# Kernel tuning notes

Measured on AMD Instinct MI355X. Metric: run time of the kernel, lower is better.

Reference implementation:

```python
import jax, jax.numpy as jnp
import numpy as np


def _conv3x3(x, w, stride=1):
    # x: [N, C_in, H, W], w: [C_out, C_in, 3, 3] (ternary {-1,0,1}), padding=1, no bias
    return jax.lax.conv_general_dilated(
        x, w,
        window_strides=(stride, stride),
        padding=((1, 1), (1, 1)),
        dimension_numbers=("NCHW", "OIHW", "NCHW"),
    )


def _bn(x, gamma, beta, mean, var, eps=1e-5):
    # inference-mode BatchNorm2d over channel dim
    inv = gamma * jax.lax.rsqrt(var + eps)
    return x * inv[None, :, None, None] + (beta - mean * inv)[None, :, None, None]


def setup_inputs() -> dict:
    key = jax.random.key(0)
    ks = jax.random.split(key, 8)
    N, C, H, W = 64, 256, 32, 32
    x = jax.random.normal(ks[0], (N, C, H, W), dtype=jnp.float32)
    # Ternary conv weights in {-1, 0, +1} (scale_and_shift=False => raw ternary values)
    w1 = jax.random.randint(ks[1], (C, C, 3, 3), -1, 2).astype(jnp.float32)
    w2 = jax.random.randint(ks[2], (C, C, 3, 3), -1, 2).astype(jnp.float32)
    # BatchNorm affine params and running stats
    g1 = jax.random.normal(ks[3], (C,), dtype=jnp.float32) * 0.1 + 1.0
    b1 = jax.random.normal(ks[4], (C,), dtype=jnp.float32) * 0.1
    g2 = jax.random.normal(ks[5], (C,), dtype=jnp.float32) * 0.1 + 1.0
    b2 = jax.random.normal(ks[6], (C,), dtype=jnp.float32) * 0.1
    rm1 = jnp.zeros((C,), dtype=jnp.float32)
    rv1 = jnp.ones((C,), dtype=jnp.float32)
    rm2 = jnp.zeros((C,), dtype=jnp.float32)
    rv2 = jnp.ones((C,), dtype=jnp.float32)
    return {"x": x, "w1": w1, "g1": g1, "b1": b1, "rm1": rm1, "rv1": rv1,
            "w2": w2, "g2": g2, "b2": b2, "rm2": rm2, "rv2": rv2}


def reference(x, w1, g1, b1, rm1, rv1, w2, g2, b2, rm2, rv2):
    # BasicBlock forward: stride=1, downsample=None -> identity skip
    h = _conv3x3(x, w1, stride=1)
    h = _bn(h, g1, b1, rm1, rv1)
    h = jax.nn.relu(h)
    h = _conv3x3(h, w2, stride=1)
    h = _bn(h, g2, b2, rm2, rv2)
    return jax.nn.relu(x + h)
```

## Files before the change

kernel.cpp:

```cpp
#include <hip/hip_runtime.h>

typedef unsigned short u16;
typedef unsigned int u32;
typedef __attribute__((ext_vector_type(8))) short bf16x8;
typedef __attribute__((ext_vector_type(4))) float f32x4;

__device__ __forceinline__ u16 f2bf(float f) {
    u32 u = __float_as_uint(f);
    u += 0x7fffu + ((u >> 16) & 1u);
    return (u16)(u >> 16);
}

__device__ __forceinline__ void llds16(void* l, const void* g) {
    __builtin_amdgcn_global_load_lds(
        (const __attribute__((address_space(1))) u32*)g,
        (__attribute__((address_space(3))) u32*)l, 16, 0, 0);
}

__global__ void prep(const float* __restrict__ x, u16* __restrict__ xt,
                     const float* __restrict__ w1, const float* __restrict__ w2,
                     u16* __restrict__ W1t, u16* __restrict__ W2t,
                     const float* __restrict__ g1, const float* __restrict__ b1,
                     const float* __restrict__ rm1, const float* __restrict__ rv1,
                     const float* __restrict__ g2, const float* __restrict__ b2,
                     const float* __restrict__ rm2, const float* __restrict__ rv2,
                     float* __restrict__ sc, u32* __restrict__ zp) {
    int t = threadIdx.x;
    int b = blockIdx.x;
    if (b < 16384) {
        __shared__ float xl[32 * 33];
        int n = b >> 8, rem = b & 255;
        int h = rem >> 3, c0 = (rem & 7) << 5;
        int cl = t >> 5, w = t & 31;
#pragma unroll
        for (int i = 0; i < 4; ++i) {
            int c = c0 + i * 8 + cl;
            xl[(i * 8 + cl) * 33 + w] = x[(n * 256 + c) * 1024 + h * 32 + w];
        }
        __syncthreads();
        int wo = t >> 3, k = t & 7;
        ushort4 o;
        o.x = f2bf(xl[(k * 4 + 0) * 33 + wo]);
        o.y = f2bf(xl[(k * 4 + 1) * 33 + wo]);
        o.z = f2bf(xl[(k * 4 + 2) * 33 + wo]);
        o.w = f2bf(xl[(k * 4 + 3) * 33 + wo]);
        *(ushort4*)&xt[((n * 32 + h) * 32 + wo) * 256 + c0 + k * 4] = o;
    } else {
        int bb = b - 16384;
        int idx = (bb & 255) * 256 + t;
        const float* src = (bb >> 8) ? w2 : w1;
        u16* dst = (bb >> 8) ? W2t : W1t;
        const float* s = src + idx * 9;
        int co = idx >> 8, ci = idx & 255;
#pragma unroll
        for (int p = 0; p < 9; ++p)
            dst[p * 65536 + co * 256 + ci] = f2bf(s[p]);
        if (bb == 0) {
            float s1 = g1[t] * rsqrtf(rv1[t] + 1e-5f);
            sc[t]       = s1;
            sc[256 + t] = b1[t] - rm1[t] * s1;
            float s2 = g2[t] * rsqrtf(rv2[t] + 1e-5f);
            sc[512 + t] = s2;
            sc[768 + t] = b2[t] - rm2[t] * s2;
            zp[t] = 0u;
            zp[t + 256] = 0u;
        }
    }
}

__global__ __launch_bounds__(512, 1) void conv_mfma(
    const u16* __restrict__ Xt,
    const u16* __restrict__ Wt,
    const float* __restrict__ sv,
    const float* __restrict__ tv,
    const float* __restrict__ skip,
    u16* __restrict__ ybf,
    float* __restrict__ yf,
    const u16* __restrict__ zp, int stage)
{
    __shared__ alignas(16) u16 ldsA[2][9 * 4 * 64 * 8];
    __shared__ alignas(16) u16 ldsB[2][40 * 64 * 8];

    int t = threadIdx.x;
    int wv = t >> 6, lane = t & 63;
    int q = lane >> 4, n16 = lane & 15;

    int bid = blockIdx.x;
    int co_t = (bid >> 3) & 3;
    int sp   = ((bid >> 5) << 3) | (bid & 7);
    int h_t  = sp & 1, nb = sp >> 1;
    int co0 = co_t << 6, h0 = h_t << 4;

    const u16* src[10];
    u32 dstOff[10];
    bool isB = (wv < 4);
    int nld = isB ? 10 : 9;
    if (isB) {
#pragma unroll
        for (int j = 0; j < 10; ++j) {
            int g2 = wv * 10 + j;
            int s = g2 * 64 + lane;
            int hi = s / 136, rem = s - hi * 136;
            int wp = rem >> 2, qq = rem & 3;
            int hin = h0 - 1 + hi;
            bool v = (wp >= 1) && (wp <= 32) && (hin >= 0) && (hin < 32);
            src[j] = v ? (Xt + (((nb << 5) + hin) * 32 + (wp - 1)) * 256 + (qq << 3))
                       : (zp + lane * 8);
            dstOff[j] = (u32)g2 << 9;
        }
    } else {
#pragma unroll
        for (int i = 0; i < 9; ++i) {
            int g = (wv - 4) * 9 + i;
            int p = g >> 2, mt = g & 3;
            src[i] = Wt + (p << 16) + ((co0 + (mt << 4) + n16) << 8) + (q << 3);
            dstOff[i] = (u32)g << 9;
        }
        src[9] = zp; dstOff[9] = 0;
    }

    f32x4 acc[4][4] = {};

    {
        u16* dst = isB ? ldsB[0] : ldsA[0];
#pragma unroll
        for (int j = 0; j < 10; ++j)
            if (j < nld) llds16(&dst[dstOff[j]], src[j]);
    }

    int c = 0;
    for (int kt = 0; kt < 8; ++kt) {
        if (kt < 7) {
            int kc = (kt + 1) << 5;
            u16* dst = isB ? ldsB[c ^ 1] : ldsA[c ^ 1];
#pragma unroll
            for (int j = 0; j < 10; ++j)
                if (j < nld) llds16(&dst[dstOff[j]], src[j] + kc);
            if (isB) asm volatile("s_waitcnt vmcnt(10)" ::: "memory");
            else     asm volatile("s_waitcnt vmcnt(9)"  ::: "memory");
        } else {
            asm volatile("s_waitcnt vmcnt(0)" ::: "memory");
        }
        __builtin_amdgcn_s_barrier();
        __builtin_amdgcn_sched_barrier(0);

        const u16* pA = ldsA[c];
        const u16* pB = ldsB[c];
        __builtin_amdgcn_s_setprio(1);
#pragma unroll
        for (int kw = 0; kw < 3; ++kw) {
            bf16x8 bFr[4][2];
#pragma unroll
            for (int r = 0; r < 4; ++r)
#pragma unroll
                for (int half = 0; half < 2; ++half) {
                    int hi = (wv << 1) + r;
                    int wp = (half << 4) + n16 + kw;
                    bFr[r][half] = *(const bf16x8*)
                        &pB[(hi * 136 + (wp << 2) + q) << 3];
                }
#pragma unroll
            for (int kh = 0; kh < 3; ++kh) {
                int p = kh * 3 + kw;
                bf16x8 aF[4];
#pragma unroll
                for (int mt = 0; mt < 4; ++mt)
                    aF[mt] = *(const bf16x8*)&pA[((p << 8) + (mt << 6) + lane) << 3];
#pragma unroll
                for (int mt = 0; mt < 4; ++mt)
#pragma unroll
                    for (int nt = 0; nt < 4; ++nt)
                        acc[mt][nt] = __builtin_amdgcn_mfma_f32_16x16x32_bf16(
                            aF[mt], bFr[(nt >> 1) + kh][nt & 1], acc[mt][nt], 0, 0, 0);
            }
        }
        __builtin_amdgcn_s_setprio(0);
        __builtin_amdgcn_sched_barrier(0);
        __builtin_amdgcn_s_barrier();
        c ^= 1;
    }

    if (stage == 1) {
#pragma unroll
        for (int mt = 0; mt < 4; ++mt) {
            int cb = co0 + (mt << 4) + (q << 2);
            f32x4 ss = *(const f32x4*)&sv[cb];
            f32x4 tt = *(const f32x4*)&tv[cb];
#pragma unroll
            for (int nt = 0; nt < 4; ++nt) {
                int h = h0 + (wv << 1) + (nt >> 1), w = ((nt & 1) << 4) + n16;
                ushort4 o;
                o.x = f2bf(fmaxf(acc[mt][nt][0] * ss[0] + tt[0], 0.f));
                o.y = f2bf(fmaxf(acc[mt][nt][1] * ss[1] + tt[1], 0.f));
                o.z = f2bf(fmaxf(acc[mt][nt][2] * ss[2] + tt[2], 0.f));
                o.w = f2bf(fmaxf(acc[mt][nt][3] * ss[3] + tt[3], 0.f));
                *(ushort4*)&ybf[(((nb << 5) + h) * 32 + w) * 256 + cb] = o;
            }
        }
    } else {
#pragma unroll
        for (int mt = 0; mt < 4; ++mt) {
            int cb = co0 + (mt << 4) + (q << 2);
            f32x4 ss = *(const f32x4*)&sv[cb];
            f32x4 tt = *(const f32x4*)&tv[cb];
#pragma unroll
            for (int nt = 0; nt < 4; ++nt) {
                int h = h0 + (wv << 1) + (nt >> 1), w = ((nt & 1) << 4) + n16;
#pragma unroll
                for (int j = 0; j < 4; ++j) {
                    int idx = (((nb << 8) + cb + j) << 10) + (h << 5) + w;
                    yf[idx] = fmaxf(acc[mt][nt][j] * ss[j] + tt[j] + skip[idx], 0.f);
                }
            }
        }
    }
}

extern "C" void kernel_launch(void* const* d_in, const int* in_sizes, int n_in,
                              void* d_out, int out_size, void* d_ws, size_t ws_size,
                              hipStream_t stream) {
    const float* x   = (const float*)d_in[0];
    const float* w1  = (const float*)d_in[1];
    const float* g1  = (const float*)d_in[2];
    const float* b1  = (const float*)d_in[3];
    const float* rm1 = (const float*)d_in[4];
    const float* rv1 = (const float*)d_in[5];
    const float* w2  = (const float*)d_in[6];
    const float* g2  = (const float*)d_in[7];
    const float* b2  = (const float*)d_in[8];
    const float* rm2 = (const float*)d_in[9];
    const float* rv2 = (const float*)d_in[10];

    char* ws = (char*)d_ws;
    u16*  XT  = (u16*)(ws);
    u16*  H1  = (u16*)(ws + 33554432);
    u16*  W1t = (u16*)(ws + 67108864);
    u16*  W2t = (u16*)(ws + 68288512);
    float* sc = (float*)(ws + 69468160);
    u32*  zpg = (u32*)(ws + 69472256);
    if (ws_size < 69474304) return;

    prep<<<16896, 256, 0, stream>>>(x, XT, w1, w2, W1t, W2t,
                                    g1, b1, rm1, rv1, g2, b2, rm2, rv2,
                                    sc, zpg);

    conv_mfma<<<512, 512, 0, stream>>>(XT, W1t, sc, sc + 256, nullptr,
                                       H1, nullptr, (const u16*)zpg, 1);
    conv_mfma<<<512, 512, 0, stream>>>(H1, W2t, sc + 512, sc + 768, x,
                                       nullptr, (float*)d_out, (const u16*)zpg, 2);
}
```

Measured before the change: 272.6 us.

## Interleave LDS prefetch with per-tap MFMA phases and allow two blocks per CU

Restructures the K loop into nine per-tap phases. Each phase loads A/B fragments, issues part of the next tile's global-to-LDS prefetch, then runs a barrier-fenced MFMA cluster, which spreads load issue across the compute. Launch bounds move to two blocks per CU to raise occupancy. The price is two extra barriers per tap, a full vmcnt(0) wait at each k-tile start, and register pressure from the occupancy target that could cause spills.

```diff
diff --git a/kernel.cpp b/kernel.cpp
--- a/kernel.cpp
+++ b/kernel.cpp
@@ -68,7 +68,7 @@
     }
 }
 
-__global__ __launch_bounds__(512, 1) void conv_mfma(
+__global__ __launch_bounds__(512, 2) void conv_mfma(
     const u16* __restrict__ Xt,
     const u16* __restrict__ Wt,
     const float* __restrict__ sv,
@@ -130,53 +130,60 @@
 
     int c = 0;
     for (int kt = 0; kt < 8; ++kt) {
-        if (kt < 7) {
-            int kc = (kt + 1) << 5;
-            u16* dst = isB ? ldsB[c ^ 1] : ldsA[c ^ 1];
-#pragma unroll
-            for (int j = 0; j < 10; ++j)
-                if (j < nld) llds16(&dst[dstOff[j]], src[j] + kc);
-            if (isB) asm volatile("s_waitcnt vmcnt(10)" ::: "memory");
-            else     asm volatile("s_waitcnt vmcnt(9)"  ::: "memory");
-        } else {
-            asm volatile("s_waitcnt vmcnt(0)" ::: "memory");
-        }
+        asm volatile("s_waitcnt vmcnt(0)" ::: "memory");
         __builtin_amdgcn_s_barrier();
-        __builtin_amdgcn_sched_barrier(0);
 
         const u16* pA = ldsA[c];
         const u16* pB = ldsB[c];
-        __builtin_amdgcn_s_setprio(1);
-#pragma unroll
-        for (int kw = 0; kw < 3; ++kw) {
-            bf16x8 bFr[4][2];
-#pragma unroll
-            for (int r = 0; r < 4; ++r)
-#pragma unroll
-                for (int half = 0; half < 2; ++half) {
-                    int hi = (wv << 1) + r;
-                    int wp = (half << 4) + n16 + kw;
-                    bFr[r][half] = *(const bf16x8*)
-                        &pB[(hi * 136 + (wp << 2) + q) << 3];
+        u16* dstS = isB ? ldsB[c ^ 1] : ldsA[c ^ 1];
+        int kc = (kt + 1) << 5;
+        bool pf = (kt < 7);
+
+        bf16x8 Bf[4][2];
+
+#pragma unroll
+        for (int tp = 0; tp < 9; ++tp) {
+            const int kw = tp / 3, kh = tp % 3;
+            const int p = kh * 3 + kw;
+            if (kh == 0) {
+#pragma unroll
+                for (int r = 0; r < 4; ++r)
+#pragma unroll
+                    for (int hf = 0; hf < 2; ++hf)
+                        Bf[r][hf] = *(const bf16x8*)
+                            &pB[((wv * 2 + r) * 136 +
+                                 (((hf << 4) + n16 + kw) << 2) + q) << 3];
+            }
+            bf16x8 Af[4];
+#pragma unroll
+            for (int mt = 0; mt < 4; ++mt)
+                Af[mt] = *(const bf16x8*)&pA[((p << 8) + (mt << 6) + lane) << 3];
+
+            if (pf && tp < 5) {
+#pragma unroll
+                for (int u = 0; u < 2; ++u) {
+                    int j = tp * 2 + u;
+                    if (j < 10) {
+                        bool go = (j < nld);
+                        if (go) llds16(&dstS[dstOff[j]], src[j] + kc);
+                    }
                 }
-#pragma unroll
-            for (int kh = 0; kh < 3; ++kh) {
-                int p = kh * 3 + kw;
-                bf16x8 aF[4];
-#pragma unroll
-                for (int mt = 0; mt < 4; ++mt)
-                    aF[mt] = *(const bf16x8*)&pA[((p << 8) + (mt << 6) + lane) << 3];
-#pragma unroll
-                for (int mt = 0; mt < 4; ++mt)
-#pragma unroll
-                    for (int nt = 0; nt < 4; ++nt)
-                        acc[mt][nt] = __builtin_amdgcn_mfma_f32_16x16x32_bf16(
-                            aF[mt], bFr[(nt >> 1) + kh][nt & 1], acc[mt][nt], 0, 0, 0);
-            }
-        }
-        __builtin_amdgcn_s_setprio(0);
-        __builtin_amdgcn_sched_barrier(0);
-        __builtin_amdgcn_s_barrier();
+            }
+
+            __builtin_amdgcn_s_barrier();
+            asm volatile("s_waitcnt lgkmcnt(0)" ::: "memory");
+            __builtin_amdgcn_sched_barrier(0);
+            __builtin_amdgcn_s_setprio(1);
+#pragma unroll
+            for (int mt = 0; mt < 4; ++mt)
+#pragma unroll
+                for (int nt = 0; nt < 4; ++nt)
+                    acc[mt][nt] = __builtin_amdgcn_mfma_f32_16x16x32_bf16(
+                        Af[mt], Bf[(nt >> 1) + kh][nt & 1], acc[mt][nt], 0, 0, 0);
+            __builtin_amdgcn_s_setprio(0);
+            __builtin_amdgcn_sched_barrier(0);
+            __builtin_amdgcn_s_barrier();
+        }
         c ^= 1;
     }
 
```

Result: no change. 275.4 us (+1.0%).

## Restructure conv K-loop: single barrier, prefetch after barrier, double-buffered LDS fragment reads

Applied to the files above, without the earlier changes.

The main loop now waits for all outstanding loads and uses one barrier per iteration instead of two. The next tile's global-to-LDS prefetch is issued after that barrier, into the buffer that was just released. The 3x3 taps are split into three kw groups whose LDS fragment reads are double-buffered in registers and separated by sched_barriers, so MFMA clusters overlap the reads for the next group. Launch bounds go to 2 blocks per CU, which caps registers per thread and may cause spills given the larger fragment arrays, while the full vmcnt(0) wait exposes global-load latency.

```diff
diff --git a/kernel.cpp b/kernel.cpp
--- a/kernel.cpp
+++ b/kernel.cpp
@@ -68,7 +68,37 @@
     }
 }
 
-__global__ __launch_bounds__(512, 1) void conv_mfma(
+#define READ_GRP(G, KW) do {                                                   \
+    _Pragma("unroll")                                                          \
+    for (int r = 0; r < 4; ++r)                                                \
+        _Pragma("unroll")                                                      \
+        for (int hf = 0; hf < 2; ++hf)                                         \
+            Bf[G][r][hf] = *(const bf16x8*)                                    \
+                &pB[((wv * 2 + r) * 136 +                                      \
+                     (((hf << 4) + n16 + (KW)) << 2) + q) << 3];               \
+    _Pragma("unroll")                                                          \
+    for (int kh = 0; kh < 3; ++kh) {                                           \
+        const int p_ = kh * 3 + (KW);                                          \
+        _Pragma("unroll")                                                      \
+        for (int mt = 0; mt < 4; ++mt)                                         \
+            Af[G][kh][mt] = *(const bf16x8*)                                   \
+                &pA[((p_ << 8) + (mt << 6) + lane) << 3];                      \
+    }                                                                          \
+} while (0)
+
+#define CLUSTER(G) do {                                                        \
+    _Pragma("unroll")                                                          \
+    for (int kh = 0; kh < 3; ++kh)                                             \
+        _Pragma("unroll")                                                      \
+        for (int mt = 0; mt < 4; ++mt)                                         \
+            _Pragma("unroll")                                                  \
+            for (int nt = 0; nt < 4; ++nt)                                     \
+                acc[mt][nt] = __builtin_amdgcn_mfma_f32_16x16x32_bf16(         \
+                    Af[G][kh][mt], Bf[G][(nt >> 1) + kh][nt & 1],              \
+                    acc[mt][nt], 0, 0, 0);                                     \
+} while (0)
+
+__global__ __launch_bounds__(512, 2) void conv_mfma(
     const u16* __restrict__ Xt,
     const u16* __restrict__ Wt,
     const float* __restrict__ sv,
@@ -130,53 +160,36 @@
 
     int c = 0;
     for (int kt = 0; kt < 8; ++kt) {
-        if (kt < 7) {
-            int kc = (kt + 1) << 5;
-            u16* dst = isB ? ldsB[c ^ 1] : ldsA[c ^ 1];
-#pragma unroll
-            for (int j = 0; j < 10; ++j)
-                if (j < nld) llds16(&dst[dstOff[j]], src[j] + kc);
-            if (isB) asm volatile("s_waitcnt vmcnt(10)" ::: "memory");
-            else     asm volatile("s_waitcnt vmcnt(9)"  ::: "memory");
-        } else {
-            asm volatile("s_waitcnt vmcnt(0)" ::: "memory");
-        }
+        asm volatile("s_waitcnt vmcnt(0)" ::: "memory");
         __builtin_amdgcn_s_barrier();
-        __builtin_amdgcn_sched_barrier(0);
 
         const u16* pA = ldsA[c];
         const u16* pB = ldsB[c];
+
+        if (kt < 7) {
+            u16* dstS = isB ? ldsB[c ^ 1] : ldsA[c ^ 1];
+            int kc = (kt + 1) << 5;
+#pragma unroll
+            for (int j = 0; j < 10; ++j)
+                if (j < nld) llds16(&dstS[dstOff[j]], src[j] + kc);
+        }
+
+        bf16x8 Bf[2][4][2];
+        bf16x8 Af[2][3][4];
+
+        READ_GRP(0, 0);
+        __builtin_amdgcn_sched_barrier(0);
+        READ_GRP(1, 1);
+        __builtin_amdgcn_sched_barrier(0);
         __builtin_amdgcn_s_setprio(1);
-#pragma unroll
-        for (int kw = 0; kw < 3; ++kw) {
-            bf16x8 bFr[4][2];
-#pragma unroll
-            for (int r = 0; r < 4; ++r)
-#pragma unroll
-                for (int half = 0; half < 2; ++half) {
-                    int hi = (wv << 1) + r;
-                    int wp = (half << 4) + n16 + kw;
-                    bFr[r][half] = *(const bf16x8*)
-                        &pB[(hi * 136 + (wp << 2) + q) << 3];
-                }
-#pragma unroll
-            for (int kh = 0; kh < 3; ++kh) {
-                int p = kh * 3 + kw;
-                bf16x8 aF[4];
-#pragma unroll
-                for (int mt = 0; mt < 4; ++mt)
-                    aF[mt] = *(const bf16x8*)&pA[((p << 8) + (mt << 6) + lane) << 3];
-#pragma unroll
-                for (int mt = 0; mt < 4; ++mt)
-#pragma unroll
-                    for (int nt = 0; nt < 4; ++nt)
-                        acc[mt][nt] = __builtin_amdgcn_mfma_f32_16x16x32_bf16(
-                            aF[mt], bFr[(nt >> 1) + kh][nt & 1], acc[mt][nt], 0, 0, 0);
-            }
-        }
+        CLUSTER(0);
+        READ_GRP(0, 2);
+        __builtin_amdgcn_sched_barrier(0);
+        CLUSTER(1);
+        __builtin_amdgcn_sched_barrier(0);
+        CLUSTER(0);
         __builtin_amdgcn_s_setprio(0);
         __builtin_amdgcn_sched_barrier(0);
-        __builtin_amdgcn_s_barrier();
         c ^= 1;
     }
 
```

Result: slower. 315.2 us (+15.6%).
